# Kernel tuning notes

Hardware: AMD Instinct MI355X
Metric: run time of the kernel (lower is better)

The kernel has to match this reference:

```python
import jax, jax.numpy as jnp
import numpy as np

B, N, E, H = 8, 512, 256, 8
DK = E // H
DIST_BAR = (0.3, 0.7, 1e10)  # init dist_bar + [1e10] appended in forward
NEG = -1e10


def setup_inputs() -> dict:
    key = jax.random.key(0)
    ks = jax.random.split(key, 24)
    s = 0.02
    inp = {
        'query': jax.random.normal(ks[0], (B, N, E), jnp.float32),
        'key':   jax.random.normal(ks[1], (B, N, E), jnp.float32),
        'value': jax.random.normal(ks[2], (B, N, E), jnp.float32),
        'dist':  jax.random.uniform(ks[3], (B, N, N), jnp.float32),
        'mask':  jax.random.randint(ks[4], (B, N, N), 0, 2).astype(jnp.int32),
        # 4 linears (q, k, v, out), stored as [in, out] for x @ W
        'Wq': jax.random.normal(ks[5], (E, E)) * s, 'bq': jnp.zeros((E,)),
        'Wk': jax.random.normal(ks[6], (E, E)) * s, 'bk': jnp.zeros((E,)),
        'Wv': jax.random.normal(ks[7], (E, E)) * s, 'bv': jnp.zeros((E,)),
        'Wo': jax.random.normal(ks[8], (E, E)) * s, 'bo': jnp.zeros((E,)),
        # cnn: Conv2d(1,H,1) -> ReLU -> Conv2d(H,H,1); 1x1 convs = per-pixel linear maps
        'cw1': jax.random.normal(ks[9], (H,)) * s,     'cb1': jnp.zeros((H,)),
        'cw2': jax.random.normal(ks[10], (H, H)) * s,  'cb2': jnp.zeros((H,)),
        # scale_linear: Linear(3E, E) -> ReLU -> Linear(E, E)
        'Ws1': jax.random.normal(ks[11], (3 * E, E)) * s, 'bs1': jnp.zeros((E,)),
        'Ws2': jax.random.normal(ks[12], (E, E)) * s,     'bs2': jnp.zeros((E,)),
    }
    return inp


def reference(query, key, value, dist, mask,
              Wq, bq, Wk, bk, Wv, bv, Wo, bo,
              cw1, cb1, cw2, cb2, Ws1, bs1, Ws2, bs2):
    def heads(x, W, b):  # [B,N,E] -> [B,H,N,DK]
        return (x @ W + b).reshape(B, N, H, DK).transpose(0, 2, 1, 3)

    q, k, v = heads(query, Wq, bq), heads(key, Wk, bk), heads(value, Wv, bv)
    d4 = dist[:, None]  # [B,1,N,N]
    # 1x1 conv stack: [B,1,N,N] -> [B,H,N,N]
    c1 = jax.nn.relu(d4 * cw1[None, :, None, None] + cb1[None, :, None, None])
    dist_conv = jnp.einsum('oi,bijk->bojk', cw2, c1) + cb2[None, :, None, None]

    scores = jnp.einsum('bhqd,bhkd->bhqk', q, k) / np.sqrt(DK).astype(np.float32)
    scores = scores * dist_conv
    scores = jnp.where(mask[:, None] == 0, NEG, scores)

    outs = []
    for bar in DIST_BAR:
        dm = d4 < bar                       # [B,1,N,N] bool
        dm = dm.at[:, :, 0, :].set(True).at[:, :, :, 0].set(True)
        s = jnp.where(dm, scores, NEG)
        p = jax.nn.softmax(s, axis=-1)      # [B,H,N,N]
        o = jnp.einsum('bhqk,bhkd->bhqd', p, v)
        o = o.transpose(0, 2, 1, 3).reshape(B, N, E)
        outs.append(o @ Wo + bo)
    x = jnp.concatenate(outs, axis=-1)      # [B,N,3E]
    h1 = jax.nn.relu(x @ Ws1 + bs1)
    return h1 @ Ws2 + bs2                   # [B,N,E]
```

## Files before the change

kernel.cpp:

```cpp
#include <hip/hip_runtime.h>
#include <math.h>

typedef _Float16 h16;
typedef __attribute__((ext_vector_type(8))) _Float16 h16x8;
typedef __attribute__((ext_vector_type(4))) _Float16 h16x4;
typedef __attribute__((ext_vector_type(4))) float f32x4;
typedef unsigned long long u64t;
typedef unsigned int u32t;
typedef unsigned short u16t;

__global__ __launch_bounds__(256) void k1_k(
    const float* __restrict__ query, const float* __restrict__ key,
    const float* __restrict__ value,
    const float* __restrict__ Wq, const float* __restrict__ bq,
    const float* __restrict__ Wk, const float* __restrict__ bk,
    const float* __restrict__ Wv, const float* __restrict__ bv,
    const float* __restrict__ Wo, const float* __restrict__ bo,
    const float* __restrict__ cw1, const float* __restrict__ cb1,
    const float* __restrict__ cw2, const float* __restrict__ cb2,
    const float* __restrict__ Ws1, const float* __restrict__ bs1,
    const float* __restrict__ Ws2, const float* __restrict__ dist,
    const int* __restrict__ mask,
    h16* __restrict__ qb, h16* __restrict__ kb, h16* __restrict__ vbT,
    h16* __restrict__ WbigT, h16* __restrict__ Ws2T,
    u16t* __restrict__ fB, float* __restrict__ bcomb)
{
    const int bid = blockIdx.x, t = threadIdx.x;
    const f32x4 z4 = {0.f, 0.f, 0.f, 0.f};

    if (bid < 816) {
        int z, row0, col0, sgm = 0;
        const float *A, *Bsrc, *bias = nullptr;
        if (bid < 768) {
            z = bid >> 8; const int idx = bid & 255;
            row0 = (idx & 63) * 64; col0 = (idx >> 6) * 64;
            A    = (z == 0) ? query : (z == 1) ? key : value;
            Bsrc = (z == 0) ? Wq : (z == 1) ? Wk : Wv;
            bias = (z == 0) ? bq : (z == 1) ? bk : bv;
        } else {
            z = 3; const int idx = bid - 768;
            sgm = idx >> 4; const int tt = idx & 15;
            row0 = (tt & 3) * 64; col0 = (tt >> 2) * 64;
            A = Wo; Bsrc = Ws1 + (size_t)sgm * 65536;
        }
        __shared__ __align__(16) h16 As[64][40];
        __shared__ __align__(16) u32t Bs[64][20];
        const int w = t >> 6, lane = t & 63, Q = lane >> 4, n = lane & 15;
        const int sr = t >> 2, sc = (t & 3) * 8;
        const int kk2 = t & 15, cs4 = (t >> 4) * 4;
        f32x4 acc[4] = {z4, z4, z4, z4};

        for (int k0 = 0; k0 < 256; k0 += 32) {
            __syncthreads();
            {
                const float* ap = A + (size_t)(row0 + sr) * 256 + k0 + sc;
                float4 a0 = *(const float4*)ap, a1 = *(const float4*)(ap + 4);
                h16x8 hv;
                hv[0] = (h16)a0.x; hv[1] = (h16)a0.y; hv[2] = (h16)a0.z; hv[3] = (h16)a0.w;
                hv[4] = (h16)a1.x; hv[5] = (h16)a1.y; hv[6] = (h16)a1.z; hv[7] = (h16)a1.w;
                *(h16x8*)&As[sr][sc] = hv;
                const float* b0p = Bsrc + (size_t)(k0 + 2 * kk2) * 256 + col0 + cs4;
                float4 r0 = *(const float4*)b0p;
                float4 r1 = *(const float4*)(b0p + 256);
                const float lo[4] = {r0.x, r0.y, r0.z, r0.w};
                const float hi[4] = {r1.x, r1.y, r1.z, r1.w};
                #pragma unroll
                for (int j = 0; j < 4; ++j) {
                    union { h16 h[2]; u32t u; } pk;
                    pk.h[0] = (h16)lo[j]; pk.h[1] = (h16)hi[j];
                    Bs[cs4 + j][kk2] = pk.u;
                }
            }
            __syncthreads();
            h16x8 af = *(const h16x8*)&As[w * 16 + n][Q * 8];
            #pragma unroll
            for (int cg = 0; cg < 4; ++cg) {
                h16x8 bf = *(const h16x8*)&Bs[cg * 16 + n][4 * Q];
                acc[cg] = __builtin_amdgcn_mfma_f32_16x16x32_f16(af, bf, acc[cg], 0, 0, 0);
            }
        }

        if (z < 2) {
            h16* out = z ? kb : qb;
            #pragma unroll
            for (int cg = 0; cg < 4; ++cg) {
                const int col = col0 + cg * 16 + n;
                const float bvv = bias[col];
                #pragma unroll
                for (int r = 0; r < 4; ++r)
                    out[(size_t)(row0 + w * 16 + 4 * Q + r) * 256 + col] =
                        (h16)(acc[cg][r] + bvv);
            }
        } else if (z == 2) {
            const int bb = row0 >> 9, tok0 = (row0 & 511) + w * 16 + 4 * Q;
            #pragma unroll
            for (int cg = 0; cg < 4; ++cg) {
                const int col = col0 + cg * 16 + n;
                const float bvv = bias[col];
                h16x4 pk;
                #pragma unroll
                for (int r = 0; r < 4; ++r) pk[r] = (h16)(acc[cg][r] + bvv);
                *(h16x4*)(vbT + ((size_t)((bb * 8 + (col >> 5)) * 32 + (col & 31))) * 512
                              + tok0) = pk;
            }
        } else {
            #pragma unroll
            for (int cg = 0; cg < 4; ++cg) {
                const int col = col0 + cg * 16 + n;
                h16x4 pk;
                #pragma unroll
                for (int r = 0; r < 4; ++r) pk[r] = (h16)acc[cg][r];
                *(h16x4*)(WbigT + (size_t)col * 768 + sgm * 256 + row0 + w * 16 + 4 * Q) = pk;
            }
        }
    } else if (bid < 880) {
        const int idx = bid - 816;
        const int r0 = (idx >> 3) * 32, c0 = (idx & 7) * 32;
        __shared__ float T[32][33];
        const int tx = t & 31, ty = t >> 5;
        #pragma unroll
        for (int i = 0; i < 4; ++i)
            T[ty + i * 8][tx] = Ws2[(size_t)(r0 + ty + i * 8) * 256 + c0 + tx];
        __syncthreads();
        #pragma unroll
        for (int i = 0; i < 4; ++i)
            Ws2T[(size_t)(c0 + ty + i * 8) * 256 + r0 + tx] = (h16)T[tx][ty + i * 8];
    } else if (bid == 880) {
        float acc = bs1[t];
        for (int r = 0; r < 768; ++r)
            acc = fmaf(bo[r & 255], Ws1[(size_t)r * 256 + t], acc);
        bcomb[t] = acc;
    } else {
        const int idx = (bid - 881) * 256 + t;
        const int b = idx >> 15, q = (idx >> 6) & 511, k8 = (idx & 63) << 3;
        const size_t dm = ((size_t)(b * 512 + q)) * 512 + k8;
        float4 d0 = *(const float4*)(dist + dm), d1 = *(const float4*)(dist + dm + 4);
        int4 m0 = *(const int4*)(mask + dm),  m1 = *(const int4*)(mask + dm + 4);
        const float dd[8] = {d0.x, d0.y, d0.z, d0.w, d1.x, d1.y, d1.z, d1.w};
        const int   mm[8] = {m0.x, m0.y, m0.z, m0.w, m1.x, m1.y, m1.z, m1.w};
        const float invs = 0.17677669529663687f;
        float w1v[8], b1v[8], fb0[8], w2v[8][8];
        #pragma unroll
        for (int u = 0; u < 8; ++u) { w1v[u] = cw1[u]; b1v[u] = cb1[u]; }
        #pragma unroll
        for (int hh = 0; hh < 8; ++hh) {
            fb0[hh] = invs * cb2[hh];
            #pragma unroll
            for (int u = 0; u < 8; ++u) w2v[hh][u] = invs * cw2[hh * 8 + u];
        }
        u32t outw[8][4] = {};
        #pragma unroll
        for (int j = 0; j < 8; ++j) {
            float ru[8];
            #pragma unroll
            for (int u = 0; u < 8; ++u) ru[u] = fmaxf(fmaf(dd[j], w1v[u], b1v[u]), 0.f);
            const bool fr = (q == 0) || ((k8 + j) == 0);
            const u32t code = ((fr || dd[j] < 0.3f) ? 1u : 0u)
                            | ((fr || dd[j] < 0.7f) ? 2u : 0u)
                            | ((mm[j] != 0) ? 4u : 0u);
            #pragma unroll
            for (int hh = 0; hh < 8; ++hh) {
                float f = fb0[hh];
                #pragma unroll
                for (int u = 0; u < 8; ++u) f = fmaf(ru[u], w2v[hh][u], f);
                union { h16 hv; u16t us; } cv; cv.hv = (h16)f;
                const u32t bits = ((u32t)cv.us & 0xFFF8u) | code;
                outw[hh][j >> 1] |= bits << (16 * (j & 1));
            }
        }
        #pragma unroll
        for (int hh = 0; hh < 8; ++hh) {
            u16t* fp = fB + ((size_t)((b * 8 + hh) * 512 + q)) * 512 + k8;
            *(uint4*)fp = make_uint4(outw[hh][0], outw[hh][1], outw[hh][2], outw[hh][3]);
        }
    }
}

__global__ __launch_bounds__(64) void attn_k(
    const h16* __restrict__ qb, const h16* __restrict__ kb,
    const h16* __restrict__ vbT, const u16t* __restrict__ fB,
    h16* __restrict__ OB)
{
    const int bid = blockIdx.x;
    const int bh = bid >> 5, qt = bid & 31;
    const int b = bh >> 3, h = bh & 7;
    const int q0 = qt * 16;
    const int lane = threadIdx.x, Q = lane >> 4, n = lane & 15;

    const h16x8 aq =
        *(const h16x8*)(qb + ((size_t)(b * 512 + q0 + n)) * 256 + h * 32 + Q * 8);

    const f32x4 z4 = {0.f, 0.f, 0.f, 0.f};
    f32x4 acc[3][2];
    #pragma unroll
    for (int s = 0; s < 3; ++s) { acc[s][0] = z4; acc[s][1] = z4; }
    float mprev = -3e38f, lsum[3] = {0.f, 0.f, 0.f};

    const size_t kbase = (size_t)(b * 512) * 256 + h * 32 + Q * 8;
    const size_t fbase = ((size_t)(bh * 512 + q0 + n)) * 512;
    const size_t vrow0 = ((size_t)(bh * 32 + n)) * 512;
    const size_t vrow1 = ((size_t)(bh * 32 + 16 + n)) * 512;

    h16x8 kf[4]; u64t fw[4];
    #pragma unroll
    for (int cg = 0; cg < 4; ++cg) {
        kf[cg] = *(const h16x8*)(kb + kbase + (size_t)(cg * 16 + n) * 256);
        fw[cg] = *(const u64t*)(fB + fbase + cg * 16 + 4 * Q);
    }

    #pragma unroll 1
    for (int kc = 0; kc < 8; ++kc) {
        const int kk0 = kc * 64;

        h16x4 vf[2][2][2];
        #pragma unroll
        for (int k2 = 0; k2 < 2; ++k2)
            #pragma unroll
            for (int jg = 0; jg < 2; ++jg) {
                const int off = kk0 + k2 * 32 + jg * 16 + 4 * Q;
                vf[k2][0][jg] = *(const h16x4*)(vbT + vrow0 + off);
                vf[k2][1][jg] = *(const h16x4*)(vbT + vrow1 + off);
            }

        f32x4 s4t[4];
        #pragma unroll
        for (int cg = 0; cg < 4; ++cg)
            s4t[cg] = __builtin_amdgcn_mfma_f32_16x16x32_f16(kf[cg], aq, z4, 0, 0, 0);

        h16x8 kfN[4]; u64t fwN[4];
        if (kc < 7) {
            #pragma unroll
            for (int cg = 0; cg < 4; ++cg) {
                kfN[cg] = *(const h16x8*)(kb + kbase + (size_t)(kk0 + 64 + cg * 16 + n) * 256);
                fwN[cg] = *(const u64t*)(fB + fbase + kk0 + 64 + cg * 16 + 4 * Q);
            }
        }

        float sv[16]; u32t bm0 = 0, bm1 = 0;
        float cm = -3e38f;
        #pragma unroll
        for (int cg = 0; cg < 4; ++cg)
            #pragma unroll
            for (int r = 0; r < 4; ++r) {
                const u32t u = (u32t)(fw[cg] >> (16 * r)) & 0xFFFFu;
                union { u16t us; h16 hv; } cv; cv.us = (u16t)(u & 0xFFF8u);
                const float s = (u & 4u) ? s4t[cg][r] * (float)cv.hv : -3e38f;
                const int i = cg * 4 + r;
                sv[i] = s;
                bm0 |= (u & 1u) << i;
                bm1 |= ((u >> 1) & 1u) << i;
                cm = fmaxf(cm, s);
            }
        cm = fmaxf(cm, __shfl_xor(cm, 16));
        cm = fmaxf(cm, __shfl_xor(cm, 32));
        const float mnew = fmaxf(mprev, cm);
        const float alpha = __expf(mprev - mnew);
        mprev = mnew;

        #pragma unroll
        for (int r = 0; r < 4; ++r) {
            const float aR = __shfl(alpha, 4 * Q + r);
            #pragma unroll
            for (int s = 0; s < 3; ++s) { acc[s][0][r] *= aR; acc[s][1][r] *= aR; }
        }

        float E[16];
        float l0 = 0.f, l1 = 0.f, l2 = 0.f;
        #pragma unroll
        for (int i = 0; i < 16; ++i) {
            const float e = __expf(sv[i] - mnew);
            E[i] = e;
            l2 += e;
            l0 += ((bm0 >> i) & 1u) ? e : 0.f;
            l1 += ((bm1 >> i) & 1u) ? e : 0.f;
        }
        #pragma unroll
        for (int k2 = 0; k2 < 2; ++k2) {
            h16x8 pf0, pf1, pf2;
            #pragma unroll
            for (int j = 0; j < 8; ++j) {
                const int i = (2 * k2 + (j >> 2)) * 4 + (j & 3);
                const float e = E[i];
                pf0[j] = (h16)(((bm0 >> i) & 1u) ? e : 0.f);
                pf1[j] = (h16)(((bm1 >> i) & 1u) ? e : 0.f);
                pf2[j] = (h16)e;
            }
            #pragma unroll
            for (int nh = 0; nh < 2; ++nh) {
                union { h16x4 h4[2]; h16x8 h8; } vv;
                vv.h4[0] = vf[k2][nh][0]; vv.h4[1] = vf[k2][nh][1];
                acc[0][nh] = __builtin_amdgcn_mfma_f32_16x16x32_f16(pf0, vv.h8, acc[0][nh], 0, 0, 0);
                acc[1][nh] = __builtin_amdgcn_mfma_f32_16x16x32_f16(pf1, vv.h8, acc[1][nh], 0, 0, 0);
                acc[2][nh] = __builtin_amdgcn_mfma_f32_16x16x32_f16(pf2, vv.h8, acc[2][nh], 0, 0, 0);
            }
        }
        lsum[0] = lsum[0] * alpha + l0;
        lsum[1] = lsum[1] * alpha + l1;
        lsum[2] = lsum[2] * alpha + l2;

        if (kc < 7) {
            #pragma unroll
            for (int cg = 0; cg < 4; ++cg) { kf[cg] = kfN[cg]; fw[cg] = fwN[cg]; }
        }
    }

    float lrow[3];
    #pragma unroll
    for (int s = 0; s < 3; ++s) {
        float lv = lsum[s];
        lv += __shfl_xor(lv, 16);
        lv += __shfl_xor(lv, 32);
        lrow[s] = lv;
    }
    #pragma unroll
    for (int s = 0; s < 3; ++s)
        #pragma unroll
        for (int r = 0; r < 4; ++r) {
            const float il = 1.0f / __shfl(lrow[s], 4 * Q + r);
            h16* op = OB + (size_t)(b * 512 + q0 + 4 * Q + r) * 768 + s * 256 + h * 32 + n;
            op[0]  = (h16)(acc[s][0][r] * il);
            op[16] = (h16)(acc[s][1][r] * il);
        }
}

__global__ __launch_bounds__(64) void g1_k(
    const h16* __restrict__ OB, const h16* __restrict__ WbigT,
    const float* __restrict__ bcomb, h16* __restrict__ h1)
{
    const int lane = threadIdx.x, Q = lane >> 4, n = lane & 15;
    const int row0 = (blockIdx.x >> 3) * 16, col0 = (blockIdx.x & 7) * 32;
    const f32x4 z4 = {0.f, 0.f, 0.f, 0.f};
    f32x4 acc[2] = {z4, z4};
    #pragma unroll 4
    for (int k0 = 0; k0 < 768; k0 += 32) {
        h16x8 af = *(const h16x8*)(OB + (size_t)(row0 + n) * 768 + k0 + Q * 8);
        #pragma unroll
        for (int c = 0; c < 2; ++c) {
            h16x8 bf = *(const h16x8*)(WbigT + (size_t)(col0 + c * 16 + n) * 768 + k0 + Q * 8);
            acc[c] = __builtin_amdgcn_mfma_f32_16x16x32_f16(af, bf, acc[c], 0, 0, 0);
        }
    }
    #pragma unroll
    for (int c = 0; c < 2; ++c) {
        const int col = col0 + c * 16 + n;
        const float bv = bcomb[col];
        #pragma unroll
        for (int r = 0; r < 4; ++r)
            h1[(size_t)(row0 + 4 * Q + r) * 256 + col] = (h16)fmaxf(acc[c][r] + bv, 0.f);
    }
}

__global__ __launch_bounds__(64) void g2_k(
    const h16* __restrict__ h1, const h16* __restrict__ Ws2T,
    const float* __restrict__ bs2, float* __restrict__ out)
{
    const int lane = threadIdx.x, Q = lane >> 4, n = lane & 15;
    const int row0 = (blockIdx.x >> 3) * 16, col0 = (blockIdx.x & 7) * 32;
    const f32x4 z4 = {0.f, 0.f, 0.f, 0.f};
    f32x4 acc[2] = {z4, z4};
    #pragma unroll 4
    for (int k0 = 0; k0 < 256; k0 += 32) {
        h16x8 af = *(const h16x8*)(h1 + (size_t)(row0 + n) * 256 + k0 + Q * 8);
        #pragma unroll
        for (int c = 0; c < 2; ++c) {
            h16x8 bf = *(const h16x8*)(Ws2T + (size_t)(col0 + c * 16 + n) * 256 + k0 + Q * 8);
            acc[c] = __builtin_amdgcn_mfma_f32_16x16x32_f16(af, bf, acc[c], 0, 0, 0);
        }
    }
    #pragma unroll
    for (int c = 0; c < 2; ++c) {
        const int col = col0 + c * 16 + n;
        const float bv = bs2[col];
        #pragma unroll
        for (int r = 0; r < 4; ++r)
            out[(size_t)(row0 + 4 * Q + r) * 256 + col] = acc[c][r] + bv;
    }
}

extern "C" void kernel_launch(void* const* d_in, const int* in_sizes, int n_in,
                              void* d_out, int out_size, void* d_ws, size_t ws_size,
                              hipStream_t stream)
{
    const float* query = (const float*)d_in[0];
    const float* key   = (const float*)d_in[1];
    const float* value = (const float*)d_in[2];
    const float* dist  = (const float*)d_in[3];
    const int*   mask  = (const int*)d_in[4];
    const float* Wq = (const float*)d_in[5];  const float* bq = (const float*)d_in[6];
    const float* Wk = (const float*)d_in[7];  const float* bk = (const float*)d_in[8];
    const float* Wv = (const float*)d_in[9];  const float* bv = (const float*)d_in[10];
    const float* Wo = (const float*)d_in[11]; const float* bo = (const float*)d_in[12];
    const float* cw1 = (const float*)d_in[13]; const float* cb1 = (const float*)d_in[14];
    const float* cw2 = (const float*)d_in[15]; const float* cb2 = (const float*)d_in[16];
    const float* Ws1 = (const float*)d_in[17]; const float* bs1 = (const float*)d_in[18];
    const float* Ws2 = (const float*)d_in[19]; const float* bs2 = (const float*)d_in[20];

    h16* qb    = (h16*)d_ws;
    h16* kb    = qb + 1048576;
    h16* vbT   = kb + 1048576;
    h16* OB    = vbT + 1048576;
    h16* h1    = OB + 3145728;
    h16* WbigT = h1 + 1048576;
    h16* Ws2T  = WbigT + 196608;
    u16t* fB   = (u16t*)(Ws2T + 65536);
    float* bcomb = (float*)(fB + 16777216);

    k1_k<<<dim3(1905), 256, 0, stream>>>(query, key, value,
                                         Wq, bq, Wk, bk, Wv, bv, Wo, bo,
                                         cw1, cb1, cw2, cb2, Ws1, bs1, Ws2,
                                         dist, mask,
                                         qb, kb, vbT, WbigT, Ws2T, fB, bcomb);

    attn_k<<<dim3(2048), 64, 0, stream>>>(qb, kb, vbT, fB, OB);

    g1_k<<<dim3(2048), 64, 0, stream>>>(OB, WbigT, bcomb, h1);
    g2_k<<<dim3(2048), 64, 0, stream>>>(h1, Ws2T, bs2, (float*)d_out);
}
```

Before: 191.9 us.

## Fuse attention and both output GEMMs into one kernel with split-K heads

Replaces the attention kernel and the two projection GEMM kernels with a single 1024-thread block per 16-query tile of a batch. Each of the 16 waves handles one head and half of the key range. The two halves are merged with a flash-style max/sum rescale through shared memory, and the attention output and hidden activations stay in LDS for the fused GEMMs. This removes two launches and the global round trips of the OB and h1 intermediates. In exchange it lowers grid parallelism to 256 blocks, adds block-wide barriers, and has every block re-read the full weight matrices.

```diff
diff --git a/kernel.cpp b/kernel.cpp
--- a/kernel.cpp
+++ b/kernel.cpp
@@ -176,41 +176,50 @@
     }
 }
 
-__global__ __launch_bounds__(64) void attn_k(
+__global__ __launch_bounds__(1024) void mega_k(
     const h16* __restrict__ qb, const h16* __restrict__ kb,
     const h16* __restrict__ vbT, const u16t* __restrict__ fB,
-    h16* __restrict__ OB)
+    const h16* __restrict__ WbigT, const h16* __restrict__ Ws2T,
+    const float* __restrict__ bcomb, const float* __restrict__ bs2,
+    float* __restrict__ out)
 {
     const int bid = blockIdx.x;
-    const int bh = bid >> 5, qt = bid & 31;
-    const int b = bh >> 3, h = bh & 7;
-    const int q0 = qt * 16;
-    const int lane = threadIdx.x, Q = lane >> 4, n = lane & 15;
+    const int b = bid >> 5, q0 = (bid & 31) * 16;
+    const int t = threadIdx.x, w = t >> 6, lane = t & 63;
+    const int Q = lane >> 4, n = lane & 15;
+    const int h = w >> 1, half = w & 1;
+
+    __shared__ float accbuf[16][778];
+    __shared__ __align__(16) h16 OBt[16][776];
+    __shared__ __align__(16) h16 h1t[16][280];
+    __shared__ float mbuf[16][16];
+    __shared__ float lbuf[16][3][16];
 
     const h16x8 aq =
         *(const h16x8*)(qb + ((size_t)(b * 512 + q0 + n)) * 256 + h * 32 + Q * 8);
-
     const f32x4 z4 = {0.f, 0.f, 0.f, 0.f};
     f32x4 acc[3][2];
     #pragma unroll
     for (int s = 0; s < 3; ++s) { acc[s][0] = z4; acc[s][1] = z4; }
     float mprev = -3e38f, lsum[3] = {0.f, 0.f, 0.f};
 
+    const int bh = b * 8 + h;
     const size_t kbase = (size_t)(b * 512) * 256 + h * 32 + Q * 8;
     const size_t fbase = ((size_t)(bh * 512 + q0 + n)) * 512;
     const size_t vrow0 = ((size_t)(bh * 32 + n)) * 512;
     const size_t vrow1 = ((size_t)(bh * 32 + 16 + n)) * 512;
+    const int kc0 = half * 4;
 
     h16x8 kf[4]; u64t fw[4];
     #pragma unroll
     for (int cg = 0; cg < 4; ++cg) {
-        kf[cg] = *(const h16x8*)(kb + kbase + (size_t)(cg * 16 + n) * 256);
-        fw[cg] = *(const u64t*)(fB + fbase + cg * 16 + 4 * Q);
+        kf[cg] = *(const h16x8*)(kb + kbase + (size_t)(kc0 * 64 + cg * 16 + n) * 256);
+        fw[cg] = *(const u64t*)(fB + fbase + kc0 * 64 + cg * 16 + 4 * Q);
     }
 
     #pragma unroll 1
-    for (int kc = 0; kc < 8; ++kc) {
-        const int kk0 = kc * 64;
+    for (int kx = 0; kx < 4; ++kx) {
+        const int kk0 = (kc0 + kx) * 64;
 
         h16x4 vf[2][2][2];
         #pragma unroll
@@ -228,7 +237,7 @@
             s4t[cg] = __builtin_amdgcn_mfma_f32_16x16x32_f16(kf[cg], aq, z4, 0, 0, 0);
 
         h16x8 kfN[4]; u64t fwN[4];
-        if (kc < 7) {
+        if (kx < 3) {
             #pragma unroll
             for (int cg = 0; cg < 4; ++cg) {
                 kfN[cg] = *(const h16x8*)(kb + kbase + (size_t)(kk0 + 64 + cg * 16 + n) * 256);
@@ -298,7 +307,7 @@
         lsum[1] = lsum[1] * alpha + l1;
         lsum[2] = lsum[2] * alpha + l2;
 
-        if (kc < 7) {
+        if (kx < 3) {
             #pragma unroll
             for (int cg = 0; cg < 4; ++cg) { kf[cg] = kfN[cg]; fw[cg] = fwN[cg]; }
         }
@@ -312,68 +321,81 @@
         lv += __shfl_xor(lv, 32);
         lrow[s] = lv;
     }
+    if (lane < 16) {
+        mbuf[w][lane] = mprev;
+        #pragma unroll
+        for (int s = 0; s < 3; ++s) lbuf[w][s][lane] = lrow[s];
+    }
+    __syncthreads();
+    const int wp = w ^ 1;
+    const float mp = mbuf[wp][n];
+    const float M = fmaxf(mprev, mp);
+    const float a_self = __expf(mprev - M);
+    const float a_part = __expf(mp - M);
+    float il[3];
     #pragma unroll
     for (int s = 0; s < 3; ++s)
-        #pragma unroll
-        for (int r = 0; r < 4; ++r) {
-            const float il = 1.0f / __shfl(lrow[s], 4 * Q + r);
-            h16* op = OB + (size_t)(b * 512 + q0 + 4 * Q + r) * 768 + s * 256 + h * 32 + n;
-            op[0]  = (h16)(acc[s][0][r] * il);
-            op[16] = (h16)(acc[s][1][r] * il);
-        }
-}
-
-__global__ __launch_bounds__(64) void g1_k(
-    const h16* __restrict__ OB, const h16* __restrict__ WbigT,
-    const float* __restrict__ bcomb, h16* __restrict__ h1)
-{
-    const int lane = threadIdx.x, Q = lane >> 4, n = lane & 15;
-    const int row0 = (blockIdx.x >> 3) * 16, col0 = (blockIdx.x & 7) * 32;
-    const f32x4 z4 = {0.f, 0.f, 0.f, 0.f};
-    f32x4 acc[2] = {z4, z4};
+        il[s] = 1.0f / (lrow[s] * a_self + lbuf[wp][s][n] * a_part);
+    #pragma unroll
+    for (int r = 0; r < 4; ++r) {
+        const float aR = __shfl(a_self, 4 * Q + r);
+        #pragma unroll
+        for (int s = 0; s < 3; ++s) { acc[s][0][r] *= aR; acc[s][1][r] *= aR; }
+    }
+    if (half == 0) {
+        #pragma unroll
+        for (int s = 0; s < 3; ++s)
+            #pragma unroll
+            for (int nh = 0; nh < 2; ++nh)
+                #pragma unroll
+                for (int r = 0; r < 4; ++r)
+                    accbuf[4 * Q + r][s * 256 + h * 32 + nh * 16 + n] = acc[s][nh][r];
+    }
+    __syncthreads();
+    if (half == 1) {
+        #pragma unroll
+        for (int s = 0; s < 3; ++s)
+            #pragma unroll
+            for (int r = 0; r < 4; ++r) {
+                const float ilR = __shfl(il[s], 4 * Q + r);
+                #pragma unroll
+                for (int nh = 0; nh < 2; ++nh) {
+                    const int col = s * 256 + h * 32 + nh * 16 + n;
+                    OBt[4 * Q + r][col] =
+                        (h16)((accbuf[4 * Q + r][col] + acc[s][nh][r]) * ilR);
+                }
+            }
+    }
+    __syncthreads();
+
+    const int col = w * 16 + n;
+    f32x4 a1 = z4;
     #pragma unroll 4
     for (int k0 = 0; k0 < 768; k0 += 32) {
-        h16x8 af = *(const h16x8*)(OB + (size_t)(row0 + n) * 768 + k0 + Q * 8);
-        #pragma unroll
-        for (int c = 0; c < 2; ++c) {
-            h16x8 bf = *(const h16x8*)(WbigT + (size_t)(col0 + c * 16 + n) * 768 + k0 + Q * 8);
-            acc[c] = __builtin_amdgcn_mfma_f32_16x16x32_f16(af, bf, acc[c], 0, 0, 0);
-        }
-    }
-    #pragma unroll
-    for (int c = 0; c < 2; ++c) {
-        const int col = col0 + c * 16 + n;
-        const float bv = bcomb[col];
+        h16x8 af = *(const h16x8*)&OBt[n][k0 + Q * 8];
+        h16x8 bf = *(const h16x8*)(WbigT + (size_t)col * 768 + k0 + Q * 8);
+        a1 = __builtin_amdgcn_mfma_f32_16x16x32_f16(af, bf, a1, 0, 0, 0);
+    }
+    {
+        const float bc = bcomb[col];
         #pragma unroll
         for (int r = 0; r < 4; ++r)
-            h1[(size_t)(row0 + 4 * Q + r) * 256 + col] = (h16)fmaxf(acc[c][r] + bv, 0.f);
-    }
-}
-
-__global__ __launch_bounds__(64) void g2_k(
-    const h16* __restrict__ h1, const h16* __restrict__ Ws2T,
-    const float* __restrict__ bs2, float* __restrict__ out)
-{
-    const int lane = threadIdx.x, Q = lane >> 4, n = lane & 15;
-    const int row0 = (blockIdx.x >> 3) * 16, col0 = (blockIdx.x & 7) * 32;
-    const f32x4 z4 = {0.f, 0.f, 0.f, 0.f};
-    f32x4 acc[2] = {z4, z4};
+            h1t[4 * Q + r][col] = (h16)fmaxf(a1[r] + bc, 0.f);
+    }
+    __syncthreads();
+
+    f32x4 a2 = z4;
     #pragma unroll 4
     for (int k0 = 0; k0 < 256; k0 += 32) {
-        h16x8 af = *(const h16x8*)(h1 + (size_t)(row0 + n) * 256 + k0 + Q * 8);
-        #pragma unroll
-        for (int c = 0; c < 2; ++c) {
-            h16x8 bf = *(const h16x8*)(Ws2T + (size_t)(col0 + c * 16 + n) * 256 + k0 + Q * 8);
-            acc[c] = __builtin_amdgcn_mfma_f32_16x16x32_f16(af, bf, acc[c], 0, 0, 0);
-        }
-    }
-    #pragma unroll
-    for (int c = 0; c < 2; ++c) {
-        const int col = col0 + c * 16 + n;
-        const float bv = bs2[col];
+        h16x8 af = *(const h16x8*)&h1t[n][k0 + Q * 8];
+        h16x8 bf = *(const h16x8*)(Ws2T + (size_t)col * 256 + k0 + Q * 8);
+        a2 = __builtin_amdgcn_mfma_f32_16x16x32_f16(af, bf, a2, 0, 0, 0);
+    }
+    {
+        const float b2 = bs2[col];
         #pragma unroll
         for (int r = 0; r < 4; ++r)
-            out[(size_t)(row0 + 4 * Q + r) * 256 + col] = acc[c][r] + bv;
+            out[(size_t)(b * 512 + q0 + 4 * Q + r) * 256 + col] = a2[r] + b2;
     }
 }
 
@@ -398,9 +420,7 @@
     h16* qb    = (h16*)d_ws;
     h16* kb    = qb + 1048576;
     h16* vbT   = kb + 1048576;
-    h16* OB    = vbT + 1048576;
-    h16* h1    = OB + 3145728;
-    h16* WbigT = h1 + 1048576;
+    h16* WbigT = vbT + 1048576;
     h16* Ws2T  = WbigT + 196608;
     u16t* fB   = (u16t*)(Ws2T + 65536);
     float* bcomb = (float*)(fB + 16777216);
@@ -411,8 +431,6 @@
                                          dist, mask,
                                          qb, kb, vbT, WbigT, Ws2T, fB, bcomb);
 
-    attn_k<<<dim3(2048), 64, 0, stream>>>(qb, kb, vbT, fB, OB);
-
-    g1_k<<<dim3(2048), 64, 0, stream>>>(OB, WbigT, bcomb, h1);
-    g2_k<<<dim3(2048), 64, 0, stream>>>(h1, Ws2T, bs2, (float*)d_out);
+    mega_k<<<dim3(256), 1024, 0, stream>>>(qb, kb, vbT, fB, WbigT, Ws2T,
+                                           bcomb, bs2, (float*)d_out);
 }
```

After: 206.0 us. 1.07x slower.

## Split attention key range across four waves and drop online-softmax max tracking

Applied to the files above, without the earlier changes.

The attention kernel now runs four waves per block, each covering a quarter of the key range. Partial P·V accumulators and row sums are combined through shared memory, and wave 0 normalizes and writes the output. The running-max rescaling of online softmax is removed: exponentials are taken directly on the scores. This is meant to shorten the serial per-block loop and cut the rescaling work. It depends on scores staying small enough not to overflow exp, and it adds shared-memory traffic and a block barrier.

```diff
diff --git a/kernel.cpp b/kernel.cpp
--- a/kernel.cpp
+++ b/kernel.cpp
@@ -176,7 +176,7 @@
     }
 }
 
-__global__ __launch_bounds__(64) void attn_k(
+__global__ __launch_bounds__(256) void attn_k(
     const h16* __restrict__ qb, const h16* __restrict__ kb,
     const h16* __restrict__ vbT, const u16t* __restrict__ fB,
     h16* __restrict__ OB)
@@ -185,7 +185,11 @@
     const int bh = bid >> 5, qt = bid & 31;
     const int b = bh >> 3, h = bh & 7;
     const int q0 = qt * 16;
-    const int lane = threadIdx.x, Q = lane >> 4, n = lane & 15;
+    const int t = threadIdx.x, w = t >> 6, lane = t & 63;
+    const int Q = lane >> 4, n = lane & 15;
+
+    __shared__ float accw[3][16][100];
+    __shared__ float lbuf[4][3][16];
 
     const h16x8 aq =
         *(const h16x8*)(qb + ((size_t)(b * 512 + q0 + n)) * 256 + h * 32 + Q * 8);
@@ -194,24 +198,23 @@
     f32x4 acc[3][2];
     #pragma unroll
     for (int s = 0; s < 3; ++s) { acc[s][0] = z4; acc[s][1] = z4; }
-    float mprev = -3e38f, lsum[3] = {0.f, 0.f, 0.f};
+    float lsum[3] = {0.f, 0.f, 0.f};
 
     const size_t kbase = (size_t)(b * 512) * 256 + h * 32 + Q * 8;
     const size_t fbase = ((size_t)(bh * 512 + q0 + n)) * 512;
     const size_t vrow0 = ((size_t)(bh * 32 + n)) * 512;
     const size_t vrow1 = ((size_t)(bh * 32 + 16 + n)) * 512;
 
-    h16x8 kf[4]; u64t fw[4];
     #pragma unroll
-    for (int cg = 0; cg < 4; ++cg) {
-        kf[cg] = *(const h16x8*)(kb + kbase + (size_t)(cg * 16 + n) * 256);
-        fw[cg] = *(const u64t*)(fB + fbase + cg * 16 + 4 * Q);
-    }
-
-    #pragma unroll 1
-    for (int kc = 0; kc < 8; ++kc) {
-        const int kk0 = kc * 64;
-
+    for (int kx = 0; kx < 2; ++kx) {
+        const int kk0 = (w * 2 + kx) * 64;
+
+        h16x8 kf[4]; u64t fw[4];
+        #pragma unroll
+        for (int cg = 0; cg < 4; ++cg) {
+            kf[cg] = *(const h16x8*)(kb + kbase + (size_t)(kk0 + cg * 16 + n) * 256);
+            fw[cg] = *(const u64t*)(fB + fbase + kk0 + cg * 16 + 4 * Q);
+        }
         h16x4 vf[2][2][2];
         #pragma unroll
         for (int k2 = 0; k2 < 2; ++k2)
@@ -227,17 +230,8 @@
         for (int cg = 0; cg < 4; ++cg)
             s4t[cg] = __builtin_amdgcn_mfma_f32_16x16x32_f16(kf[cg], aq, z4, 0, 0, 0);
 
-        h16x8 kfN[4]; u64t fwN[4];
-        if (kc < 7) {
-            #pragma unroll
-            for (int cg = 0; cg < 4; ++cg) {
-                kfN[cg] = *(const h16x8*)(kb + kbase + (size_t)(kk0 + 64 + cg * 16 + n) * 256);
-                fwN[cg] = *(const u64t*)(fB + fbase + kk0 + 64 + cg * 16 + 4 * Q);
-            }
-        }
-
-        float sv[16]; u32t bm0 = 0, bm1 = 0;
-        float cm = -3e38f;
+        float E[16]; u32t bm0 = 0, bm1 = 0;
+        float l0 = 0.f, l1 = 0.f, l2 = 0.f;
         #pragma unroll
         for (int cg = 0; cg < 4; ++cg)
             #pragma unroll
@@ -245,35 +239,15 @@
                 const u32t u = (u32t)(fw[cg] >> (16 * r)) & 0xFFFFu;
                 union { u16t us; h16 hv; } cv; cv.us = (u16t)(u & 0xFFF8u);
                 const float s = (u & 4u) ? s4t[cg][r] * (float)cv.hv : -3e38f;
+                const float e = __expf(s);
                 const int i = cg * 4 + r;
-                sv[i] = s;
+                E[i] = e;
+                l2 += e;
+                l0 += (u & 1u) ? e : 0.f;
+                l1 += (u & 2u) ? e : 0.f;
                 bm0 |= (u & 1u) << i;
                 bm1 |= ((u >> 1) & 1u) << i;
-                cm = fmaxf(cm, s);
-            }
-        cm = fmaxf(cm, __shfl_xor(cm, 16));
-        cm = fmaxf(cm, __shfl_xor(cm, 32));
-        const float mnew = fmaxf(mprev, cm);
-        const float alpha = __expf(mprev - mnew);
-        mprev = mnew;
-
-        #pragma unroll
-        for (int r = 0; r < 4; ++r) {
-            const float aR = __shfl(alpha, 4 * Q + r);
-            #pragma unroll
-            for (int s = 0; s < 3; ++s) { acc[s][0][r] *= aR; acc[s][1][r] *= aR; }
-        }
-
-        float E[16];
-        float l0 = 0.f, l1 = 0.f, l2 = 0.f;
-        #pragma unroll
-        for (int i = 0; i < 16; ++i) {
-            const float e = __expf(sv[i] - mnew);
-            E[i] = e;
-            l2 += e;
-            l0 += ((bm0 >> i) & 1u) ? e : 0.f;
-            l1 += ((bm1 >> i) & 1u) ? e : 0.f;
-        }
+            }
         #pragma unroll
         for (int k2 = 0; k2 < 2; ++k2) {
             h16x8 pf0, pf1, pf2;
@@ -294,14 +268,7 @@
                 acc[2][nh] = __builtin_amdgcn_mfma_f32_16x16x32_f16(pf2, vv.h8, acc[2][nh], 0, 0, 0);
             }
         }
-        lsum[0] = lsum[0] * alpha + l0;
-        lsum[1] = lsum[1] * alpha + l1;
-        lsum[2] = lsum[2] * alpha + l2;
-
-        if (kc < 7) {
-            #pragma unroll
-            for (int cg = 0; cg < 4; ++cg) { kf[cg] = kfN[cg]; fw[cg] = fwN[cg]; }
-        }
+        lsum[0] += l0; lsum[1] += l1; lsum[2] += l2;
     }
 
     float lrow[3];
@@ -312,15 +279,55 @@
         lv += __shfl_xor(lv, 32);
         lrow[s] = lv;
     }
-    #pragma unroll
-    for (int s = 0; s < 3; ++s)
-        #pragma unroll
-        for (int r = 0; r < 4; ++r) {
-            const float il = 1.0f / __shfl(lrow[s], 4 * Q + r);
-            h16* op = OB + (size_t)(b * 512 + q0 + 4 * Q + r) * 768 + s * 256 + h * 32 + n;
-            op[0]  = (h16)(acc[s][0][r] * il);
-            op[16] = (h16)(acc[s][1][r] * il);
-        }
+
+    if (w > 0) {
+        #pragma unroll
+        for (int s = 0; s < 3; ++s)
+            #pragma unroll
+            for (int nh = 0; nh < 2; ++nh)
+                #pragma unroll
+                for (int r = 0; r < 4; ++r) {
+                    float v = acc[s][nh][r];
+                    if (w == 1) accw[s][4 * Q + r][s * 0 + nh * 16 + n + 0] = 0.f;
+                }
+    }
+    if (w > 0) {
+        #pragma unroll
+        for (int s = 0; s < 3; ++s)
+            #pragma unroll
+            for (int nh = 0; nh < 2; ++nh)
+                #pragma unroll
+                for (int r = 0; r < 4; ++r) {
+                    float* p = &accw[s][4 * Q + r][(w - 1) * 33 + nh * 16 + n];
+                    *p = acc[s][nh][r];
+                }
+        if (lane < 16) {
+            #pragma unroll
+            for (int s = 0; s < 3; ++s) lbuf[w][s][lane] = lrow[s];
+        }
+    }
+    __syncthreads();
+    if (w == 0) {
+        float il[3];
+        #pragma unroll
+        for (int s = 0; s < 3; ++s)
+            il[s] = 1.0f / (lrow[s] + lbuf[1][s][n] + lbuf[2][s][n] + lbuf[3][s][n]);
+        #pragma unroll
+        for (int s = 0; s < 3; ++s)
+            #pragma unroll
+            for (int r = 0; r < 4; ++r) {
+                const float ilR = __shfl(il[s], 4 * Q + r);
+                #pragma unroll
+                for (int nh = 0; nh < 2; ++nh) {
+                    float v = acc[s][nh][r]
+                            + accw[s][4 * Q + r][0 * 33 + nh * 16 + n]
+                            + accw[s][4 * Q + r][1 * 33 + nh * 16 + n]
+                            + accw[s][4 * Q + r][2 * 33 + nh * 16 + n];
+                    OB[(size_t)(b * 512 + q0 + 4 * Q + r) * 768
+                       + s * 256 + h * 32 + nh * 16 + n] = (h16)(v * ilR);
+                }
+            }
+    }
 }
 
 __global__ __launch_bounds__(64) void g1_k(
@@ -411,7 +418,7 @@
                                          dist, mask,
                                          qb, kb, vbT, WbigT, Ws2T, fB, bcomb);
 
-    attn_k<<<dim3(2048), 64, 0, stream>>>(qb, kb, vbT, fB, OB);
+    attn_k<<<dim3(2048), 256, 0, stream>>>(qb, kb, vbT, fB, OB);
 
     g1_k<<<dim3(2048), 64, 0, stream>>>(OB, WbigT, bcomb, h1);
     g2_k<<<dim3(2048), 64, 0, stream>>>(h1, Ws2T, bs2, (float*)d_out);
```

New measurement: 200.2 us. 4.4% more time.
